# Performance work log

Hardware: AMD Instinct MI355X
Metric: run time of the kernel (lower is better)

The kernel has to match this reference:

```python
import jax, jax.numpy as jnp
import numpy as np
import math

B, S, H, NH = 1, 2048, 1024, 16  # batch, seq, hidden, heads


def setup_inputs() -> dict:
    key = jax.random.key(0)
    ks = jax.random.split(key, 12)
    inp = {
        "query": jax.random.normal(ks[0], (B, S, H), dtype=jnp.float32),
        "key": jax.random.normal(ks[1], (B, S, H), dtype=jnp.float32),
        "value": jax.random.normal(ks[2], (B, S, H), dtype=jnp.float32),
        "attention_mask": jax.random.randint(ks[3], (1, 1, S, S), 0, 2, dtype=jnp.int32),
        # torch nn.Linear params: y = x @ W.T + b, W init ~ U(-1/sqrt(H), 1/sqrt(H))
        "Wq": jax.random.uniform(ks[4], (H, H), jnp.float32, -1, 1) / math.sqrt(H),
        "bq": jax.random.uniform(ks[5], (H,), jnp.float32, -1, 1) / math.sqrt(H),
        "Wk": jax.random.uniform(ks[6], (H, H), jnp.float32, -1, 1) / math.sqrt(H),
        "bk": jax.random.uniform(ks[7], (H,), jnp.float32, -1, 1) / math.sqrt(H),
        "Wv": jax.random.uniform(ks[8], (H, H), jnp.float32, -1, 1) / math.sqrt(H),
        "bv": jax.random.uniform(ks[9], (H,), jnp.float32, -1, 1) / math.sqrt(H),
        "Wo": jax.random.uniform(ks[10], (H, H), jnp.float32, -1, 1) / math.sqrt(H),
        "bo": jax.random.uniform(ks[11], (H,), jnp.float32, -1, 1) / math.sqrt(H),
        "head": NH,
        "hidden_size": H,
    }
    return inp


def reference(query, key, value, attention_mask, Wq, bq, Wk, bk, Wv, bv, Wo, bo, head, hidden_size):
    b, s, _ = query.shape
    d_k = hidden_size // head

    def proj(x, W, bias):
        # [b, s, hidden] -> [b, head, s, d_k]
        y = x @ W.T + bias
        return y.reshape(b, s, head, d_k).transpose(0, 2, 1, 3)

    q = proj(query, Wq, bq)
    k = proj(key, Wk, bk)
    v = proj(value, Wv, bv)

    # naive full score matrix, as in the source (scale by sqrt(d_k) = last dim of q)
    scores = jnp.einsum("bhqd,bhkd->bhqk", q, k) / math.sqrt(d_k)
    # faithful quirk: masked positions are set to 0 (not -inf) before softmax
    scores = jnp.where(attention_mask == 0, jnp.zeros((), scores.dtype), scores)
    attn = jax.nn.softmax(scores, axis=-1)

    out = jnp.einsum("bhqk,bhkd->bhqd", attn, v)  # [b, head, s, d_k]
    out = out.transpose(0, 2, 1, 3).reshape(b, s, head * d_k)
    return out @ Wo.T + bo
```

## Files before the change

kernel.cpp:

```cpp
#include <hip/hip_runtime.h>
#include <hip/hip_bf16.h>


#define S_LEN 2048
#define HID   1024
#define NHEAD 16
#define DK    64

typedef unsigned short u16;
typedef __attribute__((ext_vector_type(8))) short bf16x8;
typedef __attribute__((ext_vector_type(4))) short bf16x4;
typedef __attribute__((ext_vector_type(4))) float f32x4;

__device__ __forceinline__ void load16_lds(const void* g, void* l) {
  __builtin_amdgcn_global_load_lds(
      (const __attribute__((address_space(1))) void*)g,
      (__attribute__((address_space(3))) void*)l, 16, 0, 0);
}

__device__ __forceinline__ short bfbits(float x) {
  __hip_bfloat16 h = __float2bfloat16(x);
  return *(short*)&h;
}
__device__ __forceinline__ bf16x8 cvt8(float4 a, float4 b) {
  bf16x8 r;
  r[0] = bfbits(a.x); r[1] = bfbits(a.y); r[2] = bfbits(a.z); r[3] = bfbits(a.w);
  r[4] = bfbits(b.x); r[5] = bfbits(b.y); r[6] = bfbits(b.z); r[7] = bfbits(b.w);
  return r;
}
__device__ __forceinline__ float bf2f(u16 u) {
  unsigned v = (unsigned)u << 16;
  return *(float*)&v;
}

__global__ __launch_bounds__(256) void cvt_kernel(
    const float* __restrict__ q, const float* __restrict__ k,
    const float* __restrict__ v, const float* __restrict__ wq,
    const float* __restrict__ wk, const float* __restrict__ wv,
    const float* __restrict__ wo, u16* __restrict__ Xbf,
    u16* __restrict__ Wbf) {
  const int y = blockIdx.y;
  size_t i = ((size_t)blockIdx.x * 256 + threadIdx.x) * 8;
  const float* src;
  u16* dst;
  size_t n;
  if (y < 3) {
    src = y == 0 ? q : (y == 1 ? k : v);
    dst = Xbf + (size_t)y * (S_LEN * HID);
    n = (size_t)S_LEN * HID;
  } else {
    int w = y - 3;
    src = w == 0 ? wq : (w == 1 ? wk : (w == 2 ? wv : wo));
    dst = Wbf + (size_t)w * (HID * HID);
    n = (size_t)HID * HID;
  }
  if (i >= n) return;
  float4 a = *(const float4*)(src + i);
  float4 b = *(const float4*)(src + i + 4);
  *(bf16x8*)(dst + i) = cvt8(a, b);
}

__global__ void pack_mask_kernel(const int* __restrict__ mask,
                                 unsigned int* __restrict__ bits) {
  int w = blockIdx.x * blockDim.x + threadIdx.x;
  const int4* p = (const int4*)(mask + (size_t)w * 32);
  unsigned word = 0;
#pragma unroll
  for (int i = 0; i < 8; ++i) {
    int4 v = p[i];
    word |= (unsigned)(v.x != 0) << (i * 4 + 0);
    word |= (unsigned)(v.y != 0) << (i * 4 + 1);
    word |= (unsigned)(v.z != 0) << (i * 4 + 2);
    word |= (unsigned)(v.w != 0) << (i * 4 + 3);
  }
  bits[w] = word;
}

__global__ __launch_bounds__(256) void gemm_qkv(
    const u16* __restrict__ Xbf, const u16* __restrict__ Wbf,
    const float* __restrict__ bq, const float* __restrict__ bk,
    const float* __restrict__ bv, u16* __restrict__ Qb,
    u16* __restrict__ Kb, u16* __restrict__ Vt) {
  constexpr int Mm = 2048, Nn = 1024, Kk = 1024, NIT = 16;
  const int z = blockIdx.z;
  const u16* A = Xbf + (size_t)z * (S_LEN * HID);
  const u16* W = Wbf + (size_t)z * (HID * HID);
  const float* bias = z == 0 ? bq : (z == 1 ? bk : bv);
  u16* C = z == 0 ? Qb : (z == 1 ? Kb : Vt);
  const float oscale = (z == 0) ? 0.125f : 1.0f;
  const int transpose = (z == 2);

  const int tid = threadIdx.x, lane = tid & 63, wave = tid >> 6;
  const int q4 = lane >> 4, c16 = lane & 15;
  const int bx = blockIdx.x;
  const int mBase = (bx & 31) * 64;
  const int nBase = (bx >> 5) * 128;
  const int wn = wave * 32;

  __shared__ __align__(16) u16 As[2][2][64 * 32];
  __shared__ __align__(16) u16 Bs[2][2][128 * 32];

  f32x4 acc[4][2] = {};
  const int srow = lane >> 2, se8 = (lane & 3) * 8;

  auto issue = [&](int it, int buf) {
#pragma unroll
    for (int j = 0; j < 2; ++j) {
      int u = wave * 2 + j, h = u >> 2, grp = u & 3;
      load16_lds(A + (size_t)(mBase + grp * 16 + srow) * Kk + it * 64 +
                     h * 32 + se8,
                 &As[buf][h][grp * 512]);
    }
#pragma unroll
    for (int j = 0; j < 4; ++j) {
      int u = wave * 4 + j, h = u >> 3, grp = u & 7;
      load16_lds(W + (size_t)(nBase + grp * 16 + srow) * Kk + it * 64 +
                     h * 32 + se8,
                 &Bs[buf][h][grp * 512]);
    }
  };

  issue(0, 0);
  __syncthreads();

  for (int it = 0; it < NIT; ++it) {
    const int buf = it & 1, nbuf = buf ^ 1;
    if (it + 1 < NIT) issue(it + 1, nbuf);
#pragma unroll
    for (int kk = 0; kk < 2; ++kk) {
      bf16x8 af[4], bfr[2];
#pragma unroll
      for (int t = 0; t < 4; ++t)
        af[t] = *(const bf16x8*)&As[buf][kk][(t * 16 + c16) * 32 + q4 * 8];
#pragma unroll
      for (int t = 0; t < 2; ++t)
        bfr[t] = *(const bf16x8*)&Bs[buf][kk][(wn + t * 16 + c16) * 32 + q4 * 8];
#pragma unroll
      for (int mt = 0; mt < 4; ++mt)
#pragma unroll
        for (int nt = 0; nt < 2; ++nt)
          acc[mt][nt] = __builtin_amdgcn_mfma_f32_16x16x32_bf16(
              af[mt], bfr[nt], acc[mt][nt], 0, 0, 0);
    }
    __syncthreads();
  }

#pragma unroll
  for (int nt = 0; nt < 2; ++nt) {
    int col = nBase + wn + nt * 16 + c16;
    float bv2 = bias[col];
#pragma unroll
    for (int mt = 0; mt < 4; ++mt) {
#pragma unroll
      for (int r = 0; r < 4; ++r) {
        int row = mBase + mt * 16 + q4 * 4 + r;
        float v = (acc[mt][nt][r] + bv2) * oscale;
        if (transpose)
          ((__hip_bfloat16*)C)[(size_t)col * Mm + row] = __float2bfloat16(v);
        else
          ((__hip_bfloat16*)C)[(size_t)row * Nn + col] = __float2bfloat16(v);
      }
    }
  }
}

__global__ __launch_bounds__(512) void attn_kernel(
    const u16* __restrict__ Qb, const u16* __restrict__ Kb,
    const u16* __restrict__ Vt, const unsigned* __restrict__ mbits,
    u16* __restrict__ partO, float* __restrict__ partL) {
  constexpr int NITA = S_LEN / 2 / 64;
  const int qt = blockIdx.x, h = blockIdx.y, zz = blockIdx.z;
  const int tid = threadIdx.x, lane = tid & 63, wave = tid >> 6;
  const int q4 = lane >> 4, c16 = lane & 15;

  __shared__ __align__(16) u16 Ks[2][2][64 * 32];
  __shared__ __align__(16) u16 Vs[2][2][64 * 32];
  __shared__ __align__(16) u16 Ps[8][16 * 72];

  const int wq0 = qt * 128 + wave * 16;

  bf16x8 qf[2];
#pragma unroll
  for (int kk = 0; kk < 2; ++kk)
    qf[kk] = *(const bf16x8*)(Qb + (size_t)(wq0 + c16) * HID + h * DK +
                              kk * 32 + q4 * 8);

  f32x4 o[4] = {};
  float l_lane[4] = {};

  const int srow = lane >> 2;
  const int se8  = (lane & 3) * 8;
  const int kvbase = zz * (S_LEN / 2);

  auto issueKV = [&](int it, int buf) {
    const int kv0 = kvbase + it * 64;
#pragma unroll
    for (int j = 0; j < 2; ++j) {
      int i = wave * 2 + j;
      if (i < 8) {
        int half = i >> 2, grp = i & 3;
        load16_lds(Kb + (size_t)(kv0 + grp * 16 + srow) * HID + h * DK +
                       half * 32 + se8,
                   &Ks[buf][half][grp * 512]);
      } else {
        int ii = i - 8;
        int half = ii >> 2, grp = ii & 3;
        load16_lds(Vt + (size_t)(h * DK + grp * 16 + srow) * S_LEN + kv0 +
                       half * 32 + se8,
                   &Vs[buf][half][grp * 512]);
      }
    }
  };

  issueKV(0, 0);
  __syncthreads();

  for (int it = 0; it < NITA; ++it) {
    const int buf = it & 1, nbuf = buf ^ 1;
    const int kv0 = kvbase + it * 64;
    if (it + 1 < NITA) issueKV(it + 1, nbuf);

    f32x4 sv[4];
#pragma unroll
    for (int nt = 0; nt < 4; ++nt) {
      bf16x8 kf0 = *(const bf16x8*)&Ks[buf][0][(nt * 16 + c16) * 32 + q4 * 8];
      bf16x8 kf1 = *(const bf16x8*)&Ks[buf][1][(nt * 16 + c16) * 32 + q4 * 8];
      f32x4 a = {};
      a = __builtin_amdgcn_mfma_f32_16x16x32_bf16(qf[0], kf0, a, 0, 0, 0);
      a = __builtin_amdgcn_mfma_f32_16x16x32_bf16(qf[1], kf1, a, 0, 0, 0);
      sv[nt] = a;
    }

#pragma unroll
    for (int r = 0; r < 4; ++r) {
      int row = wq0 + q4 * 4 + r;
      const unsigned* mrow = mbits + (size_t)row * 64 + (kv0 >> 5);
      unsigned w0 = mrow[0], w1 = mrow[1];
#pragma unroll
      for (int nt = 0; nt < 4; ++nt) {
        unsigned word = (nt < 2) ? w0 : w1;
        int bit = ((nt & 1) * 16) + c16;
        float s = ((word >> bit) & 1u) ? sv[nt][r] : 0.0f;
        float p = __expf(s);
        sv[nt][r] = p;
        l_lane[r] += p;
      }
    }

    u16* pw = &Ps[wave][0];
#pragma unroll
    for (int r = 0; r < 4; ++r)
#pragma unroll
      for (int nt = 0; nt < 4; ++nt)
        ((__hip_bfloat16*)pw)[(q4 * 4 + r) * 72 + nt * 16 + c16] =
            __float2bfloat16(sv[nt][r]);
    asm volatile("s_waitcnt lgkmcnt(0)" ::: "memory");

#pragma unroll
    for (int kk = 0; kk < 2; ++kk) {
      bf16x8 pa = *(const bf16x8*)&pw[c16 * 72 + kk * 32 + q4 * 8];
#pragma unroll
      for (int nt = 0; nt < 4; ++nt) {
        bf16x8 vb = *(const bf16x8*)&Vs[buf][kk][(nt * 16 + c16) * 32 + q4 * 8];
        o[nt] = __builtin_amdgcn_mfma_f32_16x16x32_bf16(pa, vb, o[nt], 0, 0, 0);
      }
    }
    __syncthreads();
  }

#pragma unroll
  for (int r = 0; r < 4; ++r) {
    float s = l_lane[r];
#pragma unroll
    for (int d = 1; d < 16; d <<= 1) s += __shfl_xor(s, d);
    l_lane[r] = s;
  }

#pragma unroll
  for (int r = 0; r < 4; ++r) {
    int row = wq0 + q4 * 4 + r;
#pragma unroll
    for (int nt = 0; nt < 4; ++nt)
      ((__hip_bfloat16*)partO)[((size_t)zz * S_LEN + row) * HID + h * DK +
                               nt * 16 + c16] = __float2bfloat16(o[nt][r]);
    if (c16 == 0)
      partL[((size_t)zz * NHEAD + h) * S_LEN + row] = l_lane[r];
  }
}

__global__ __launch_bounds__(256) void combine_kernel(
    const u16* __restrict__ partO, const float* __restrict__ partL,
    u16* __restrict__ ctx) {
  size_t idx = ((size_t)blockIdx.x * 256 + threadIdx.x) * 4;
  int row = (int)(idx >> 10);
  int col = (int)(idx & 1023);
  int h = col >> 6;
  float l = partL[(size_t)h * S_LEN + row] +
            partL[((size_t)NHEAD + h) * S_LEN + row];
  float inv = 1.0f / l;
  bf16x4 a = *(const bf16x4*)(partO + idx);
  bf16x4 b = *(const bf16x4*)(partO + (size_t)S_LEN * HID + idx);
  bf16x4 r;
#pragma unroll
  for (int j = 0; j < 4; ++j) {
    float v = (bf2f((u16)a[j]) + bf2f((u16)b[j])) * inv;
    r[j] = bfbits(v);
  }
  *(bf16x4*)(ctx + idx) = r;
}

__global__ __launch_bounds__(256) void gemm_out(
    const u16* __restrict__ ctx, const u16* __restrict__ Wo,
    const float* __restrict__ bo, float* __restrict__ out) {
  constexpr int Nn = 1024, Kk = 1024, NIT = 16;
  const int tid = threadIdx.x, lane = tid & 63, wave = tid >> 6;
  const int q4 = lane >> 4, c16 = lane & 15;
  const int bx = blockIdx.x;
  const int mBase = (bx & 63) * 32;
  const int nBase = (bx >> 6) * 128;
  const int wn = wave * 32;

  __shared__ __align__(16) u16 As[2][2][32 * 32];
  __shared__ __align__(16) u16 Bs[2][2][128 * 32];

  f32x4 acc[2][2] = {};
  const int srow = lane >> 2, se8 = (lane & 3) * 8;

  auto issue = [&](int it, int buf) {
    {
      int u = wave, h = u >> 1, grp = u & 1;
      load16_lds(ctx + (size_t)(mBase + grp * 16 + srow) * Kk + it * 64 +
                     h * 32 + se8,
                 &As[buf][h][grp * 512]);
    }
#pragma unroll
    for (int j = 0; j < 4; ++j) {
      int u = wave * 4 + j, h = u >> 3, grp = u & 7;
      load16_lds(Wo + (size_t)(nBase + grp * 16 + srow) * Kk + it * 64 +
                     h * 32 + se8,
                 &Bs[buf][h][grp * 512]);
    }
  };

  issue(0, 0);
  __syncthreads();

  for (int it = 0; it < NIT; ++it) {
    const int buf = it & 1, nbuf = buf ^ 1;
    if (it + 1 < NIT) issue(it + 1, nbuf);
#pragma unroll
    for (int kk = 0; kk < 2; ++kk) {
      bf16x8 af[2], bfr[2];
#pragma unroll
      for (int t = 0; t < 2; ++t)
        af[t] = *(const bf16x8*)&As[buf][kk][(t * 16 + c16) * 32 + q4 * 8];
#pragma unroll
      for (int t = 0; t < 2; ++t)
        bfr[t] = *(const bf16x8*)&Bs[buf][kk][(wn + t * 16 + c16) * 32 + q4 * 8];
#pragma unroll
      for (int mt = 0; mt < 2; ++mt)
#pragma unroll
        for (int nt = 0; nt < 2; ++nt)
          acc[mt][nt] = __builtin_amdgcn_mfma_f32_16x16x32_bf16(
              af[mt], bfr[nt], acc[mt][nt], 0, 0, 0);
    }
    __syncthreads();
  }

#pragma unroll
  for (int nt = 0; nt < 2; ++nt) {
    int col = nBase + wn + nt * 16 + c16;
    float bv = bo[col];
#pragma unroll
    for (int mt = 0; mt < 2; ++mt)
#pragma unroll
      for (int r = 0; r < 4; ++r) {
        int row = mBase + mt * 16 + q4 * 4 + r;
        out[(size_t)row * Nn + col] = acc[mt][nt][r] + bv;
      }
  }
}

extern "C" void kernel_launch(void* const* d_in, const int* in_sizes, int n_in,
                              void* d_out, int out_size, void* d_ws, size_t ws_size,
                              hipStream_t stream) {
  const float* q    = (const float*)d_in[0];
  const float* k    = (const float*)d_in[1];
  const float* v    = (const float*)d_in[2];
  const int*   mask = (const int*)d_in[3];
  const float* Wq = (const float*)d_in[4];
  const float* bq = (const float*)d_in[5];
  const float* Wk = (const float*)d_in[6];
  const float* bk = (const float*)d_in[7];
  const float* Wv = (const float*)d_in[8];
  const float* bv = (const float*)d_in[9];
  const float* Wo = (const float*)d_in[10];
  const float* bo = (const float*)d_in[11];

  const size_t M2 = (size_t)S_LEN * HID;
  const size_t W1 = (size_t)HID * HID;
  const size_t need = (4 * W1 + 3 * M2 + 3 * M2) * 2 +
                      (size_t)S_LEN * 64 * 4 + 2 * NHEAD * S_LEN * 4;
  if (ws_size < need) return;

  u16* Wbf = (u16*)d_ws;
  u16* Xbf = Wbf + 4 * W1;
  u16* partO = Xbf;
  u16* Qb = Xbf + 3 * M2;
  u16* Kb = Qb + M2;
  u16* Vt = Kb + M2;
  unsigned* mbits = (unsigned*)(Vt + M2);
  float* partL = (float*)(mbits + (size_t)S_LEN * 64);
  u16* ctx = Qb;

  hipLaunchKernelGGL(cvt_kernel, dim3(1024, 7), dim3(256), 0, stream,
                     q, k, v, Wq, Wk, Wv, Wo, Xbf, Wbf);

  hipLaunchKernelGGL(pack_mask_kernel, dim3((S_LEN * (S_LEN / 32)) / 256),
                     dim3(256), 0, stream, mask, mbits);

  hipLaunchKernelGGL(gemm_qkv, dim3(256, 1, 3), dim3(256), 0, stream,
                     Xbf, Wbf, bq, bk, bv, Qb, Kb, Vt);

  hipLaunchKernelGGL(attn_kernel, dim3(S_LEN / 128, NHEAD, 2), dim3(512), 0,
                     stream, Qb, Kb, Vt, mbits, partO, partL);

  hipLaunchKernelGGL(combine_kernel, dim3((S_LEN * HID / 4) / 256), dim3(256),
                     0, stream, partO, partL, ctx);

  hipLaunchKernelGGL(gemm_out, dim3(512), dim3(256), 0, stream,
                     ctx, Wbf + 3 * W1, bo, (float*)d_out);
}
```

Measured before the change: 202.5 us.

## Fuse activation bf16 conversion into QKV GEMM, use exp2, shrink attention blocks

```diff
diff --git a/kernel.cpp b/kernel.cpp
--- a/kernel.cpp
+++ b/kernel.cpp
@@ -33,31 +33,16 @@
   return *(float*)&v;
 }
 
-__global__ __launch_bounds__(256) void cvt_kernel(
-    const float* __restrict__ q, const float* __restrict__ k,
-    const float* __restrict__ v, const float* __restrict__ wq,
-    const float* __restrict__ wk, const float* __restrict__ wv,
-    const float* __restrict__ wo, u16* __restrict__ Xbf,
+__global__ __launch_bounds__(256) void cvtW_kernel(
+    const float* __restrict__ wq, const float* __restrict__ wk,
+    const float* __restrict__ wv, const float* __restrict__ wo,
     u16* __restrict__ Wbf) {
   const int y = blockIdx.y;
+  const float* src = y == 0 ? wq : (y == 1 ? wk : (y == 2 ? wv : wo));
   size_t i = ((size_t)blockIdx.x * 256 + threadIdx.x) * 8;
-  const float* src;
-  u16* dst;
-  size_t n;
-  if (y < 3) {
-    src = y == 0 ? q : (y == 1 ? k : v);
-    dst = Xbf + (size_t)y * (S_LEN * HID);
-    n = (size_t)S_LEN * HID;
-  } else {
-    int w = y - 3;
-    src = w == 0 ? wq : (w == 1 ? wk : (w == 2 ? wv : wo));
-    dst = Wbf + (size_t)w * (HID * HID);
-    n = (size_t)HID * HID;
-  }
-  if (i >= n) return;
   float4 a = *(const float4*)(src + i);
   float4 b = *(const float4*)(src + i + 4);
-  *(bf16x8*)(dst + i) = cvt8(a, b);
+  *(bf16x8*)(Wbf + (size_t)y * (HID * HID) + i) = cvt8(a, b);
 }
 
 __global__ void pack_mask_kernel(const int* __restrict__ mask,
@@ -77,17 +62,18 @@
 }
 
 __global__ __launch_bounds__(256) void gemm_qkv(
-    const u16* __restrict__ Xbf, const u16* __restrict__ Wbf,
+    const float* __restrict__ qf32, const float* __restrict__ kf32,
+    const float* __restrict__ vf32, const u16* __restrict__ Wbf,
     const float* __restrict__ bq, const float* __restrict__ bk,
     const float* __restrict__ bv, u16* __restrict__ Qb,
     u16* __restrict__ Kb, u16* __restrict__ Vt) {
   constexpr int Mm = 2048, Nn = 1024, Kk = 1024, NIT = 16;
   const int z = blockIdx.z;
-  const u16* A = Xbf + (size_t)z * (S_LEN * HID);
+  const float* A = z == 0 ? qf32 : (z == 1 ? kf32 : vf32);
   const u16* W = Wbf + (size_t)z * (HID * HID);
   const float* bias = z == 0 ? bq : (z == 1 ? bk : bv);
   u16* C = z == 0 ? Qb : (z == 1 ? Kb : Vt);
-  const float oscale = (z == 0) ? 0.125f : 1.0f;
+  const float oscale = (z == 0) ? 0.125f * 1.4426950408889634f : 1.0f;
   const int transpose = (z == 2);
 
   const int tid = threadIdx.x, lane = tid & 63, wave = tid >> 6;
@@ -103,14 +89,7 @@
   f32x4 acc[4][2] = {};
   const int srow = lane >> 2, se8 = (lane & 3) * 8;
 
-  auto issue = [&](int it, int buf) {
-#pragma unroll
-    for (int j = 0; j < 2; ++j) {
-      int u = wave * 2 + j, h = u >> 2, grp = u & 3;
-      load16_lds(A + (size_t)(mBase + grp * 16 + srow) * Kk + it * 64 +
-                     h * 32 + se8,
-                 &As[buf][h][grp * 512]);
-    }
+  auto issueW = [&](int it, int buf) {
 #pragma unroll
     for (int j = 0; j < 4; ++j) {
       int u = wave * 4 + j, h = u >> 3, grp = u & 7;
@@ -119,13 +98,37 @@
                  &Bs[buf][h][grp * 512]);
     }
   };
-
-  issue(0, 0);
+  float4 ar[2][2];
+  auto loadA = [&](int it) {
+#pragma unroll
+    for (int j = 0; j < 2; ++j) {
+      int u = wave * 2 + j, h = u >> 2, grp = u & 3;
+      const float* s = A + (size_t)(mBase + grp * 16 + srow) * Kk + it * 64 +
+                       h * 32 + se8;
+      ar[j][0] = *(const float4*)s;
+      ar[j][1] = *(const float4*)(s + 4);
+    }
+  };
+  auto storeA = [&](int buf) {
+#pragma unroll
+    for (int j = 0; j < 2; ++j) {
+      int u = wave * 2 + j, h = u >> 2, grp = u & 3;
+      *(bf16x8*)&As[buf][h][grp * 512 + srow * 32 + se8] =
+          cvt8(ar[j][0], ar[j][1]);
+    }
+  };
+
+  loadA(0);
+  storeA(0);
+  issueW(0, 0);
   __syncthreads();
 
   for (int it = 0; it < NIT; ++it) {
     const int buf = it & 1, nbuf = buf ^ 1;
-    if (it + 1 < NIT) issue(it + 1, nbuf);
+    if (it + 1 < NIT) {
+      issueW(it + 1, nbuf);
+      loadA(it + 1);
+    }
 #pragma unroll
     for (int kk = 0; kk < 2; ++kk) {
       bf16x8 af[4], bfr[2];
@@ -142,6 +145,7 @@
           acc[mt][nt] = __builtin_amdgcn_mfma_f32_16x16x32_bf16(
               af[mt], bfr[nt], acc[mt][nt], 0, 0, 0);
     }
+    if (it + 1 < NIT) storeA(nbuf);
     __syncthreads();
   }
 
@@ -164,7 +168,7 @@
   }
 }
 
-__global__ __launch_bounds__(512) void attn_kernel(
+__global__ __launch_bounds__(256) void attn_kernel(
     const u16* __restrict__ Qb, const u16* __restrict__ Kb,
     const u16* __restrict__ Vt, const unsigned* __restrict__ mbits,
     u16* __restrict__ partO, float* __restrict__ partL) {
@@ -175,9 +179,9 @@
 
   __shared__ __align__(16) u16 Ks[2][2][64 * 32];
   __shared__ __align__(16) u16 Vs[2][2][64 * 32];
-  __shared__ __align__(16) u16 Ps[8][16 * 72];
-
-  const int wq0 = qt * 128 + wave * 16;
+  __shared__ __align__(16) u16 Ps[4][16 * 72];
+
+  const int wq0 = qt * 64 + wave * 16;
 
   bf16x8 qf[2];
 #pragma unroll
@@ -195,8 +199,8 @@
   auto issueKV = [&](int it, int buf) {
     const int kv0 = kvbase + it * 64;
 #pragma unroll
-    for (int j = 0; j < 2; ++j) {
-      int i = wave * 2 + j;
+    for (int j = 0; j < 4; ++j) {
+      int i = wave * 4 + j;
       if (i < 8) {
         int half = i >> 2, grp = i & 3;
         load16_lds(Kb + (size_t)(kv0 + grp * 16 + srow) * HID + h * DK +
@@ -241,7 +245,7 @@
         unsigned word = (nt < 2) ? w0 : w1;
         int bit = ((nt & 1) * 16) + c16;
         float s = ((word >> bit) & 1u) ? sv[nt][r] : 0.0f;
-        float p = __expf(s);
+        float p = exp2f(s);
         sv[nt][r] = p;
         l_lane[r] += p;
       }
@@ -399,30 +403,29 @@
 
   const size_t M2 = (size_t)S_LEN * HID;
   const size_t W1 = (size_t)HID * HID;
-  const size_t need = (4 * W1 + 3 * M2 + 3 * M2) * 2 +
+  const size_t need = (4 * W1 + 2 * M2 + 3 * M2) * 2 +
                       (size_t)S_LEN * 64 * 4 + 2 * NHEAD * S_LEN * 4;
   if (ws_size < need) return;
 
   u16* Wbf = (u16*)d_ws;
-  u16* Xbf = Wbf + 4 * W1;
-  u16* partO = Xbf;
-  u16* Qb = Xbf + 3 * M2;
+  u16* partO = Wbf + 4 * W1;
+  u16* Qb = partO + 2 * M2;
   u16* Kb = Qb + M2;
   u16* Vt = Kb + M2;
   unsigned* mbits = (unsigned*)(Vt + M2);
   float* partL = (float*)(mbits + (size_t)S_LEN * 64);
   u16* ctx = Qb;
 
-  hipLaunchKernelGGL(cvt_kernel, dim3(1024, 7), dim3(256), 0, stream,
-                     q, k, v, Wq, Wk, Wv, Wo, Xbf, Wbf);
+  hipLaunchKernelGGL(cvtW_kernel, dim3(512, 4), dim3(256), 0, stream,
+                     Wq, Wk, Wv, Wo, Wbf);
 
   hipLaunchKernelGGL(pack_mask_kernel, dim3((S_LEN * (S_LEN / 32)) / 256),
                      dim3(256), 0, stream, mask, mbits);
 
   hipLaunchKernelGGL(gemm_qkv, dim3(256, 1, 3), dim3(256), 0, stream,
-                     Xbf, Wbf, bq, bk, bv, Qb, Kb, Vt);
-
-  hipLaunchKernelGGL(attn_kernel, dim3(S_LEN / 128, NHEAD, 2), dim3(512), 0,
+                     q, k, v, Wbf, bq, bk, bv, Qb, Kb, Vt);
+
+  hipLaunchKernelGGL(attn_kernel, dim3(S_LEN / 64, NHEAD, 2), dim3(256), 0,
                      stream, Qb, Kb, Vt, mbits, partO, partL);
 
   hipLaunchKernelGGL(combine_kernel, dim3((S_LEN * HID / 4) / 256), dim3(256),
```

New measurement: 213.4 us. 5.4% more time.
